# Kernel optimization log

Hardware: AMD Instinct MI355X
Metric: run time of the kernel (lower is better)

## Reference

```python
import jax, jax.numpy as jnp
import numpy as np

EPS = 1e-7  # keras backend epsilon

def setup_inputs() -> dict:
    key = jax.random.key(0)
    k1, k2, k3, k4, k5 = jax.random.split(key, 5)
    B, S, D, A = 64, 2048, 512, 256
    x = jax.random.normal(k1, (B, S, D), dtype=jnp.float32)
    mask = jax.random.randint(k2, (B, S), 0, 2) > 0
    # keras 'normal' initializer: RandomNormal(stddev=0.05)
    W = 0.05 * jax.random.normal(k3, (D, A), dtype=jnp.float32)
    b = 0.05 * jax.random.normal(k4, (A,), dtype=jnp.float32)
    u = 0.05 * jax.random.normal(k5, (A, 1), dtype=jnp.float32)
    return {"x": x, "mask": mask, "W": W, "b": b, "u": u}

def reference(x, mask, W, b, u):
    # x: [B,S,D], W: [D,A], b: [A], u: [A,1]
    uit = jnp.tanh(jnp.einsum('bsd,da->bsa', x, W) + b)   # [B,S,A]
    ait = jnp.einsum('bsa,a->bs', uit, u[:, 0])           # [B,S]
    ait = jnp.exp(ait)
    ait = ait * mask.astype(x.dtype)
    ait = ait / (jnp.sum(ait, axis=1, keepdims=True) + EPS)  # [B,S]
    return jnp.einsum('bsd,bs->bd', x, ait)               # [B,D]
```

## Files before the change

kernel.cpp:

```cpp
#include <hip/hip_runtime.h>
#include <stdint.h>

#define B_ 64
#define S_ 2048
#define D_ 512
#define A_ 256
#define TM 32
#define TPB 16
#define NBLK 256
#define EPS 1e-7f

typedef short bf16x8 __attribute__((ext_vector_type(8)));
typedef float f32x4  __attribute__((ext_vector_type(4)));

#define WS_WT   0
#define WS_PART 262144
#define WS_ZP   786432
#define WS_FLAG 787456

__device__ __forceinline__ uint32_t f32pair_to_bf16(float a, float b) {
  uint32_t ua = __float_as_uint(a), ub = __float_as_uint(b);
  ua = (ua + 0x7fffu + ((ua >> 16) & 1u)) >> 16;
  ub = (ub + 0x7fffu + ((ub >> 16) & 1u)) & 0xffff0000u;
  return ua | ub;
}

__device__ __forceinline__ void gload_lds16(const float* g, float* l) {
  __builtin_amdgcn_global_load_lds(
      (const __attribute__((address_space(1))) uint32_t*)g,
      (__attribute__((address_space(3))) uint32_t*)l, 16, 0, 0);
}

__device__ __forceinline__ float row16_sum(float x) {
  int v = __float_as_int(x);
  x += __int_as_float(__builtin_amdgcn_update_dpp(v, v, 0xB1, 0xF, 0xF, false));
  v = __float_as_int(x);
  x += __int_as_float(__builtin_amdgcn_update_dpp(v, v, 0x4E, 0xF, 0xF, false));
  v = __float_as_int(x);
  x += __int_as_float(__builtin_amdgcn_update_dpp(v, v, 0x141, 0xF, 0xF, false));
  v = __float_as_int(x);
  x += __int_as_float(__builtin_amdgcn_update_dpp(v, v, 0x128, 0xF, 0xF, false));
  return x;
}

__global__ __launch_bounds__(256) void prep_kernel(
    const float* __restrict__ W, const void* __restrict__ mask,
    uint16_t* __restrict__ Wt, int* __restrict__ flag)
{
  int i = blockIdx.x * 256 + threadIdx.x;
  if (i < A_ * D_) {
    int a = i >> 9;
    int d = i & (D_ - 1);
    uint32_t u = __float_as_uint(W[d * A_ + a]);
    u = (u + 0x7fffu + ((u >> 16) & 1u)) >> 16;
    Wt[i] = (uint16_t)u;
  }
  if (blockIdx.x == 0 && threadIdx.x < 64) {
    const uint32_t* mw = (const uint32_t*)mask;
    int hit = 0;
    for (int k = 0; k < 16; ++k) {
      uint32_t v = mw[threadIdx.x + 64 * k];
      uint32_t b0 = v & 0xff, b1 = (v >> 8) & 0xff, b2 = (v >> 16) & 0xff, b3 = v >> 24;
      if (b0 <= 1u && b1 <= 1u && b2 <= 1u && b3 <= 1u && (b1 | b2 | b3)) hit = 1;
    }
    hit = __any(hit);
    if (threadIdx.x == 0) *flag = hit ? 1 : 0;
  }
}

__global__ __launch_bounds__(512, 2) void att_main(
    const float* __restrict__ x, const void* __restrict__ mask,
    const float* __restrict__ bias, const float* __restrict__ uvec,
    const uint16_t* __restrict__ Wt, float* __restrict__ part,
    float* __restrict__ Zpart, const int* __restrict__ flag)
{
  __shared__ float xf[TM * D_];
  __shared__ uint16_t xs[2][TM * D_];
  __shared__ float sp[8][TM];
  __shared__ float me[TM * TPB];

  const int tid = threadIdx.x;
  const int l  = tid & 63, w  = tid >> 6;
  const int lr = l & 15,   lg = l >> 4;
  const int bx = blockIdx.x;
  const int b  = bx >> 2;
  const int s0 = (bx & 3) * (TM * TPB);
  const float* xb = x + ((size_t)b * S_ + s0) * D_;
  const int mflag = *flag;

  {
    int midx = b * S_ + s0 + tid;
    int mv = mflag ? (((const unsigned char*)mask)[midx] != 0)
                   : (((const int*)mask)[midx] != 0);
    me[tid] = mv ? 1.0f : 0.0f;
  }

  bf16x8 bfr[32];
  {
    const uint16_t* wtb = Wt + (size_t)(w * 32 + lr) * D_;
    #pragma unroll
    for (int ks = 0; ks < 16; ++ks)
      #pragma unroll
      for (int nt = 0; nt < 2; ++nt)
        bfr[ks * 2 + nt] = *(const bf16x8*)(wtb + nt * 16 * D_ + ks * 32 + lg * 8);
  }
  float bn[2], un[2];
  #pragma unroll
  for (int nt = 0; nt < 2; ++nt) {
    int n = w * 32 + nt * 16 + lr;
    bn[nt] = bias[n];
    un[nt] = uvec[n];
  }

  float num_acc = 0.0f;
  float zacc    = 0.0f;

  #pragma unroll
  for (int i = 0; i < 8; ++i) {
    int id = w * 8 + i, row = id >> 1, h = id & 1;
    gload_lds16(xb + row * D_ + (2 * l + h) * 4, &xf[row * D_ + h * 256]);
  }
  __syncthreads();

  #pragma unroll
  for (int c = 0; c < 4; ++c) {
    int row = c * 8 + w;
    float4 lo = *(const float4*)&xf[row * D_ + l * 4];
    float4 hi = *(const float4*)&xf[row * D_ + 256 + l * 4];
    uint4 pk;
    pk.x = f32pair_to_bf16(lo.x, lo.y);
    pk.y = f32pair_to_bf16(lo.z, lo.w);
    pk.z = f32pair_to_bf16(hi.x, hi.y);
    pk.w = f32pair_to_bf16(hi.z, hi.w);
    *(uint4*)(&xs[0][row * D_ + ((l ^ (row & 7)) * 8)]) = pk;
  }
  __syncthreads();

  {
    const float* xt = xb + (size_t)TM * D_;
    #pragma unroll
    for (int i = 0; i < 8; ++i) {
      int id = w * 8 + i, row = id >> 1, h = id & 1;
      gload_lds16(xt + row * D_ + (2 * l + h) * 4, &xf[row * D_ + h * 256]);
    }
  }

  #pragma unroll 2
  for (int t = 0; t < TPB; ++t) {
    const uint16_t* buf = xs[t & 1];

    f32x4 acc[2][2];
    #pragma unroll
    for (int mt = 0; mt < 2; ++mt)
      #pragma unroll
      for (int nt = 0; nt < 2; ++nt)
        acc[mt][nt] = (f32x4){0.f, 0.f, 0.f, 0.f};

    #pragma unroll
    for (int ks = 0; ks < 16; ++ks) {
      bf16x8 af[2];
      #pragma unroll
      for (int mt = 0; mt < 2; ++mt)
        af[mt] = *(const bf16x8*)(&buf[(mt * 16 + lr) * D_ + (((ks * 4 + lg) ^ (lr & 7)) * 8)]);
      #pragma unroll
      for (int mt = 0; mt < 2; ++mt)
        #pragma unroll
        for (int nt = 0; nt < 2; ++nt)
          acc[mt][nt] = __builtin_amdgcn_mfma_f32_16x16x32_bf16(af[mt], bfr[ks * 2 + nt], acc[mt][nt], 0, 0, 0);
    }

    #pragma unroll
    for (int mt = 0; mt < 2; ++mt) {
      #pragma unroll
      for (int r = 0; r < 4; ++r) {
        float ssum = 0.0f;
        #pragma unroll
        for (int nt = 0; nt < 2; ++nt) {
          float vv = acc[mt][nt][r] + bn[nt];
          float av = fabsf(vv);
          float e2 = __expf(-2.0f * av);
          float th = 1.0f - 2.0f * e2 * __builtin_amdgcn_rcpf(1.0f + e2);
          ssum += copysignf(th, vv) * un[nt];
        }
        ssum = row16_sum(ssum);
        if (lr == 0) sp[w][mt * 16 + lg * 4 + r] = ssum;
      }
    }
    __syncthreads();

    if (t + 1 < TPB) {
      uint16_t* nb = xs[(t + 1) & 1];
      #pragma unroll
      for (int c = 0; c < 4; ++c) {
        int row = c * 8 + w;
        float4 lo = *(const float4*)&xf[row * D_ + l * 4];
        float4 hi = *(const float4*)&xf[row * D_ + 256 + l * 4];
        uint4 pk;
        pk.x = f32pair_to_bf16(lo.x, lo.y);
        pk.y = f32pair_to_bf16(lo.z, lo.w);
        pk.z = f32pair_to_bf16(hi.x, hi.y);
        pk.w = f32pair_to_bf16(hi.z, hi.w);
        *(uint4*)(&nb[row * D_ + ((l ^ (row & 7)) * 8)]) = pk;
      }
    }

    float eval = 0.0f;
    if (l < 32) {
      float sc = 0.0f;
      #pragma unroll
      for (int ww = 0; ww < 8; ++ww) sc += sp[ww][l];
      eval = me[t * TM + l] * __expf(sc);
    }
    if (w == 0 && l < 32) {
      float tot = eval;
      tot += __shfl_xor(tot, 1);
      tot += __shfl_xor(tot, 2);
      tot += __shfl_xor(tot, 4);
      tot += __shfl_xor(tot, 8);
      tot += __shfl_xor(tot, 16);
      if (l == 0) zacc += tot;
    }

    {
      int cw = tid >> 3, wo = (tid & 7) >> 1;
      #pragma unroll
      for (int s = 0; s < TM; ++s) {
        float e = __int_as_float(__builtin_amdgcn_readlane(__float_as_int(eval), s));
        uint32_t vv = *(const uint32_t*)(&buf[s * D_ + (cw ^ (s & 7)) * 8 + wo * 2]);
        float xv = (tid & 1) ? __uint_as_float(vv & 0xffff0000u)
                             : __uint_as_float(vv << 16);
        num_acc = fmaf(e, xv, num_acc);
      }
    }
    __syncthreads();

    if (t + 2 < TPB) {
      const float* xt = xb + (size_t)(t + 2) * TM * D_;
      #pragma unroll
      for (int i = 0; i < 8; ++i) {
        int id = w * 8 + i, row = id >> 1, h = id & 1;
        gload_lds16(xt + row * D_ + (2 * l + h) * 4, &xf[row * D_ + h * 256]);
      }
    }
  }

  part[(size_t)bx * D_ + tid] = num_acc;
  if (tid == 0) Zpart[bx] = zacc;
}

__global__ __launch_bounds__(256) void scale_kernel(
    const float* __restrict__ part, const float* __restrict__ Zpart,
    float* __restrict__ out)
{
  int idx = blockIdx.x * 256 + threadIdx.x;
  int b = idx >> 9;
  int d = idx & (D_ - 1);
  float s = 0.0f, z = 0.0f;
  #pragma unroll
  for (int g = 0; g < 4; ++g) {
    s += part[(size_t)(b * 4 + g) * D_ + d];
    z += Zpart[b * 4 + g];
  }
  out[idx] = s / (z + EPS);
}

extern "C" void kernel_launch(void* const* d_in, const int* in_sizes, int n_in,
                              void* d_out, int out_size, void* d_ws, size_t ws_size,
                              hipStream_t stream)
{
  const float* x    = (const float*)d_in[0];
  const void*  mask = d_in[1];
  const float* W    = (const float*)d_in[2];
  const float* bias = (const float*)d_in[3];
  const float* u    = (const float*)d_in[4];
  float* out = (float*)d_out;

  char* ws = (char*)d_ws;
  uint16_t* Wt  = (uint16_t*)(ws + WS_WT);
  float* part   = (float*)(ws + WS_PART);
  float* Zpart  = (float*)(ws + WS_ZP);
  int*   flag   = (int*)(ws + WS_FLAG);

  prep_kernel<<<(A_ * D_ + 255) / 256, 256, 0, stream>>>(W, mask, Wt, flag);
  att_main<<<NBLK, 512, 0, stream>>>(x, mask, bias, u, Wt, part, Zpart, flag);
  scale_kernel<<<(B_ * D_ + 255) / 256, 256, 0, stream>>>(part, Zpart, out);
}
```

Before: 372.0 us.

## Replace block barriers with LDS atomic counter soft barriers and per-wave row ownership

Result: slower. 395.7 us (+6.4%).

```diff
diff --git a/kernel.cpp b/kernel.cpp
--- a/kernel.cpp
+++ b/kernel.cpp
@@ -9,6 +9,9 @@
 #define TPB 16
 #define NBLK 256
 #define EPS 1e-7f
+
+#define WAIT_LGKM0 0xC07F
+#define WAIT_VM0   0x0F70
 
 typedef short bf16x8 __attribute__((ext_vector_type(8)));
 typedef float f32x4  __attribute__((ext_vector_type(4)));
@@ -41,6 +44,16 @@
   v = __float_as_int(x);
   x += __int_as_float(__builtin_amdgcn_update_dpp(v, v, 0x128, 0xF, 0xF, false));
   return x;
+}
+
+__device__ __forceinline__ void soft_bar(int* cnt, int target) {
+  __builtin_amdgcn_sched_barrier(0);
+  __builtin_amdgcn_s_waitcnt(WAIT_LGKM0);
+  if ((threadIdx.x & 63) == 0)
+    __hip_atomic_fetch_add(cnt, 1, __ATOMIC_RELAXED, __HIP_MEMORY_SCOPE_WORKGROUP);
+  while (__hip_atomic_load(cnt, __ATOMIC_RELAXED, __HIP_MEMORY_SCOPE_WORKGROUP) < target)
+    __builtin_amdgcn_s_sleep(1);
+  __builtin_amdgcn_sched_barrier(0);
 }
 
 __global__ __launch_bounds__(256) void prep_kernel(
@@ -78,6 +91,7 @@
   __shared__ uint16_t xs[2][TM * D_];
   __shared__ float sp[8][TM];
   __shared__ float me[TM * TPB];
+  __shared__ int bcnt;
 
   const int tid = threadIdx.x;
   const int l  = tid & 63, w  = tid >> 6;
@@ -86,6 +100,11 @@
   const int b  = bx >> 2;
   const int s0 = (bx & 3) * (TM * TPB);
   const float* xb = x + ((size_t)b * S_ + s0) * D_;
+
+  if (tid == 0) bcnt = 0;
+  __syncthreads();
+  int bt = 8;
+
   const int mflag = *flag;
 
   {
@@ -117,14 +136,13 @@
 
   #pragma unroll
   for (int i = 0; i < 8; ++i) {
-    int id = w * 8 + i, row = id >> 1, h = id & 1;
+    int row = w * 4 + (i >> 1), h = i & 1;
     gload_lds16(xb + row * D_ + (2 * l + h) * 4, &xf[row * D_ + h * 256]);
   }
-  __syncthreads();
-
+  __builtin_amdgcn_s_waitcnt(WAIT_VM0);
   #pragma unroll
   for (int c = 0; c < 4; ++c) {
-    int row = c * 8 + w;
+    int row = w * 4 + c;
     float4 lo = *(const float4*)&xf[row * D_ + l * 4];
     float4 hi = *(const float4*)&xf[row * D_ + 256 + l * 4];
     uint4 pk;
@@ -134,16 +152,17 @@
     pk.w = f32pair_to_bf16(hi.z, hi.w);
     *(uint4*)(&xs[0][row * D_ + ((l ^ (row & 7)) * 8)]) = pk;
   }
-  __syncthreads();
-
+  __builtin_amdgcn_sched_barrier(0);
+  __builtin_amdgcn_s_waitcnt(WAIT_LGKM0);
   {
     const float* xt = xb + (size_t)TM * D_;
     #pragma unroll
     for (int i = 0; i < 8; ++i) {
-      int id = w * 8 + i, row = id >> 1, h = id & 1;
+      int row = w * 4 + (i >> 1), h = i & 1;
       gload_lds16(xt + row * D_ + (2 * l + h) * 4, &xf[row * D_ + h * 256]);
     }
   }
+  soft_bar(&bcnt, bt); bt += 8;
 
   #pragma unroll 2
   for (int t = 0; t < TPB; ++t) {
@@ -186,13 +205,44 @@
         if (lr == 0) sp[w][mt * 16 + lg * 4 + r] = ssum;
       }
     }
-    __syncthreads();
+
+    soft_bar(&bcnt, bt); bt += 8;
+
+    float eval = 0.0f;
+    if (l < 32) {
+      float sc = 0.0f;
+      #pragma unroll
+      for (int ww = 0; ww < 8; ++ww) sc += sp[ww][l];
+      eval = me[t * TM + l] * __expf(sc);
+    }
+    if (w == 0 && l < 32) {
+      float tot = eval;
+      tot += __shfl_xor(tot, 1);
+      tot += __shfl_xor(tot, 2);
+      tot += __shfl_xor(tot, 4);
+      tot += __shfl_xor(tot, 8);
+      tot += __shfl_xor(tot, 16);
+      if (l == 0) zacc += tot;
+    }
+
+    {
+      int cw = tid >> 3, wo = (tid & 7) >> 1;
+      #pragma unroll
+      for (int s = 0; s < TM; ++s) {
+        float e = __int_as_float(__builtin_amdgcn_readlane(__float_as_int(eval), s));
+        uint32_t vv = *(const uint32_t*)(&buf[s * D_ + (cw ^ (s & 7)) * 8 + wo * 2]);
+        float xv = (tid & 1) ? __uint_as_float(vv & 0xffff0000u)
+                             : __uint_as_float(vv << 16);
+        num_acc = fmaf(e, xv, num_acc);
+      }
+    }
 
     if (t + 1 < TPB) {
+      __builtin_amdgcn_s_waitcnt(WAIT_VM0);
       uint16_t* nb = xs[(t + 1) & 1];
       #pragma unroll
       for (int c = 0; c < 4; ++c) {
-        int row = c * 8 + w;
+        int row = w * 4 + c;
         float4 lo = *(const float4*)&xf[row * D_ + l * 4];
         float4 hi = *(const float4*)&xf[row * D_ + 256 + l * 4];
         uint4 pk;
@@ -202,46 +252,19 @@
         pk.w = f32pair_to_bf16(hi.z, hi.w);
         *(uint4*)(&nb[row * D_ + ((l ^ (row & 7)) * 8)]) = pk;
       }
-    }
-
-    float eval = 0.0f;
-    if (l < 32) {
-      float sc = 0.0f;
-      #pragma unroll
-      for (int ww = 0; ww < 8; ++ww) sc += sp[ww][l];
-      eval = me[t * TM + l] * __expf(sc);
-    }
-    if (w == 0 && l < 32) {
-      float tot = eval;
-      tot += __shfl_xor(tot, 1);
-      tot += __shfl_xor(tot, 2);
-      tot += __shfl_xor(tot, 4);
-      tot += __shfl_xor(tot, 8);
-      tot += __shfl_xor(tot, 16);
-      if (l == 0) zacc += tot;
-    }
-
-    {
-      int cw = tid >> 3, wo = (tid & 7) >> 1;
-      #pragma unroll
-      for (int s = 0; s < TM; ++s) {
-        float e = __int_as_float(__builtin_amdgcn_readlane(__float_as_int(eval), s));
-        uint32_t vv = *(const uint32_t*)(&buf[s * D_ + (cw ^ (s & 7)) * 8 + wo * 2]);
-        float xv = (tid & 1) ? __uint_as_float(vv & 0xffff0000u)
-                             : __uint_as_float(vv << 16);
-        num_acc = fmaf(e, xv, num_acc);
+      __builtin_amdgcn_sched_barrier(0);
+      __builtin_amdgcn_s_waitcnt(WAIT_LGKM0);
+      if (t + 2 < TPB) {
+        const float* xt = xb + (size_t)(t + 2) * TM * D_;
+        #pragma unroll
+        for (int i = 0; i < 8; ++i) {
+          int row = w * 4 + (i >> 1), h = i & 1;
+          gload_lds16(xt + row * D_ + (2 * l + h) * 4, &xf[row * D_ + h * 256]);
+        }
       }
     }
-    __syncthreads();
-
-    if (t + 2 < TPB) {
-      const float* xt = xb + (size_t)(t + 2) * TM * D_;
-      #pragma unroll
-      for (int i = 0; i < 8; ++i) {
-        int id = w * 8 + i, row = id >> 1, h = id & 1;
-        gload_lds16(xt + row * D_ + (2 * l + h) * 4, &xf[row * D_ + h * 256]);
-      }
-    }
+
+    soft_bar(&bcnt, bt); bt += 8;
   }
 
   part[(size_t)bx * D_ + tid] = num_acc;
```
